# Kernel optimization log

Measured on AMD Instinct MI355X. Metric: run time of the kernel, lower is better.

The kernel has to match this reference:

```python
import jax, jax.numpy as jnp
import numpy as np
from jax import lax


def setup_inputs() -> dict:
    key = jax.random.key(0)
    ks = jax.random.split(key, 9)
    B, C, H, W = 32, 16, 128, 128
    x = jax.random.normal(ks[0], (B, C, H, W), dtype=jnp.float32)
    # sobel_x kernel as in source; the executed code leaves conv_sobel_x with tiled sobel_x.T
    sobel = jnp.array([[-1.0, 0.0, 1.0], [-2.0, 0.0, 2.0], [-1.0, 0.0, 1.0]], dtype=jnp.float32) / 8.0
    Wx = jnp.tile(sobel.T, (16, 16, 1, 1))  # [O=16, I=16, 3, 3]
    bx = jax.random.normal(ks[1], (16,), dtype=jnp.float32) * 0.05
    # conv_sobel_y retained its default (random) init in the source; model as random params
    Wy = jax.random.normal(ks[2], (16, 16, 3, 3), dtype=jnp.float32) * (1.0 / np.sqrt(16 * 9))
    by = jax.random.normal(ks[3], (16,), dtype=jnp.float32) * 0.05
    W1 = jax.random.normal(ks[4], (128, 48), dtype=jnp.float32) * (1.0 / np.sqrt(48))
    b1 = jax.random.normal(ks[5], (128,), dtype=jnp.float32) * 0.01
    W2 = jax.random.normal(ks[6], (16, 128), dtype=jnp.float32) * (1.0 / np.sqrt(128))
    b2 = jax.random.normal(ks[7], (16,), dtype=jnp.float32) * 0.01
    return {"x": x, "Wx": Wx, "bx": bx, "Wy": Wy, "by": by,
            "W1": W1, "b1": b1, "W2": W2, "b2": b2}


def _conv_same(x, w, b):
    # x: [B,C,H,W], w: [O,I,3,3] -> [B,O,H,W]
    y = lax.conv_general_dilated(x, w, window_strides=(1, 1), padding="SAME",
                                 dimension_numbers=("NCHW", "OIHW", "NCHW"))
    return y + b[None, :, None, None]


def reference(x, Wx, bx, Wy, by, W1, b1, W2, b2):
    # concat along channels: [B, 48, H, W]
    feat = jnp.concatenate([_conv_same(x, Wx, bx), _conv_same(x, Wy, by), x], axis=1)
    # torch transpose(1, 3): [B, W, H, 48]
    feat = jnp.transpose(feat, (0, 3, 2, 1))
    h = jax.nn.relu(jnp.einsum("bwhc,oc->bwho", feat, W1) + b1)
    out = jnp.einsum("bwhc,oc->bwho", h, W2) + b2  # [B, W, H, 16]
    return out
```

## Files before the change

### kernel.cpp

```cpp
#include <hip/hip_runtime.h>
#include <hip/hip_bf16.h>

typedef __hip_bfloat16 bf16;
typedef __attribute__((ext_vector_type(8))) short short8;
typedef __attribute__((ext_vector_type(4))) short short4v;
typedef __attribute__((ext_vector_type(4))) float float4v;

#define TH 16
#define TW 8
#define HALO_H 18
#define HALO_W 10
#define CS 24
#define KS 136

#define W2B_EL 20480
#define WSF_BYTE 45056

__global__ void prep(const float* __restrict__ Wx, const float* __restrict__ bx,
                     const float* __restrict__ Wy, const float* __restrict__ by,
                     const float* __restrict__ W1, const float* __restrict__ b1,
                     const float* __restrict__ W2, const float* __restrict__ b2,
                     bf16* __restrict__ wsb, float* __restrict__ wsf) {
    int t = blockIdx.x * blockDim.x + threadIdx.x;
    int stride = gridDim.x * blockDim.x;
    for (int f = t; f < 128 * 160; f += stride) {
        int j = f / 160, k = f - j * 160;
        int g = k >> 4, c = k & 15;
        float v = 0.0f;
        if (g < 9) {
            for (int o = 0; o < 16; ++o) {
                float wx = Wx[(o * 16 + c) * 9 + g];
                float wy = Wy[(o * 16 + c) * 9 + g];
                v = fmaf(W1[j * 48 + o], wx, v);
                v = fmaf(W1[j * 48 + 16 + o], wy, v);
            }
            if (g == 4) v += W1[j * 48 + 32 + c];
        }
        wsb[f] = __float2bfloat16(v);
    }
    for (int f = t; f < 2048; f += stride) wsb[W2B_EL + f] = __float2bfloat16(W2[f]);
    for (int j = t; j < 128; j += stride) {
        float v = b1[j];
        for (int o = 0; o < 16; ++o) {
            v = fmaf(W1[j * 48 + o], bx[o], v);
            v = fmaf(W1[j * 48 + 16 + o], by[o], v);
        }
        wsf[j] = v;
    }
    if (t < 16) wsf[128 + t] = b2[t];
}

__global__ __launch_bounds__(256, 2) void nca_mfma(const float* __restrict__ x,
                                                   const bf16* __restrict__ wsb,
                                                   const float* __restrict__ wsf,
                                                   float* __restrict__ out,
                                                   int gridTiles) {
    __shared__ bf16 xs[HALO_W * HALO_H * CS];
    __shared__ bf16 hs[128 * KS];

    const int tid = threadIdx.x;
    const int wave = tid >> 6;
    const int lane = tid & 63;
    const int hl = lane & 15;
    const int quad = lane >> 4;
    const int r0 = quad * 4;
    const int mgrp = wave >> 1;
    const int ngrp = wave & 1;

    short8 afrag[4][5];
#pragma unroll
    for (int mt = 0; mt < 4; ++mt) {
        int m = mgrp * 64 + mt * 16 + hl;
#pragma unroll
        for (int q = 0; q < 5; ++q)
            afrag[mt][q] = *(const short8*)(wsb + m * 160 + q * 32 + quad * 8);
    }
    short8 w2frag[4];
#pragma unroll
    for (int r = 0; r < 4; ++r)
        w2frag[r] = *(const short8*)(wsb + W2B_EL + hl * 128 + r * 32 + quad * 8);
    float b1r[4][4];
#pragma unroll
    for (int mt = 0; mt < 4; ++mt)
#pragma unroll
        for (int r = 0; r < 4; ++r) b1r[mt][r] = wsf[mgrp * 64 + mt * 16 + r0 + r];
    float b2r[4];
#pragma unroll
    for (int r = 0; r < 4; ++r) b2r[r] = wsf[128 + r0 + r];

    for (int t = blockIdx.x; t < 4096; t += gridTiles) {
        int b = t >> 7;
        int rem = t & 127;
        int wt = rem >> 3, ht = rem & 7;
        int h0 = ht * 16, w0 = wt * 8;

        __syncthreads();

        const float* xb = x + (size_t)b * 16 * 128 * 128;
        for (int f = tid; f < 16 * HALO_H * HALO_W; f += 256) {
            int c = f / (HALO_H * HALO_W);
            int rr = f - c * (HALO_H * HALO_W);
            int hh = rr / HALO_W;
            int ww = rr - hh * HALO_W;
            int gh = h0 - 1 + hh, gw = w0 - 1 + ww;
            float v = 0.0f;
            if ((unsigned)gh < 128u && (unsigned)gw < 128u)
                v = xb[(c * 128 + gh) * 128 + gw];
            xs[(ww * HALO_H + hh) * CS + c] = __float2bfloat16(v);
        }
        __syncthreads();

        float4v acc[4][4];
#pragma unroll
        for (int mt = 0; mt < 4; ++mt)
#pragma unroll
            for (int nt = 0; nt < 4; ++nt) acc[mt][nt] = (float4v)0.0f;

#pragma unroll
        for (int q = 0; q < 5; ++q) {
            int g = q * 2 + (quad >> 1);
            if (g > 8) g = 8;
            int kh = g / 3, kw = g - kh * 3;
            int c0 = (quad & 1) * 8;
            short8 bfrag[4];
#pragma unroll
            for (int nt = 0; nt < 4; ++nt) {
                int ww = ngrp * 4 + nt + kw;
                bfrag[nt] = *(const short8*)(xs + (ww * HALO_H + hl + kh) * CS + c0);
            }
#pragma unroll
            for (int nt = 0; nt < 4; ++nt)
#pragma unroll
                for (int mt = 0; mt < 4; ++mt)
                    acc[mt][nt] = __builtin_amdgcn_mfma_f32_16x16x32_bf16(
                        afrag[mt][q], bfrag[nt], acc[mt][nt], 0, 0, 0);
        }

#pragma unroll
        for (int mt = 0; mt < 4; ++mt)
#pragma unroll
            for (int nt = 0; nt < 4; ++nt) {
                int p = (ngrp * 4 + nt) * 16 + hl;
                int m = mgrp * 64 + mt * 16 + r0;
                short4v pk;
#pragma unroll
                for (int r = 0; r < 4; ++r) {
                    float v = acc[mt][nt][r] + b1r[mt][r];
                    v = fmaxf(v, 0.0f);
                    bf16 hb = __float2bfloat16(v);
                    pk[r] = *reinterpret_cast<short*>(&hb);
                }
                *(short4v*)(hs + p * KS + m) = pk;
            }
        __syncthreads();

        float4v acc2[2];
        acc2[0] = (float4v)0.0f;
        acc2[1] = (float4v)0.0f;
#pragma unroll
        for (int r = 0; r < 4; ++r) {
#pragma unroll
            for (int i = 0; i < 2; ++i) {
                int p = (wave * 2 + i) * 16 + hl;
                short8 bfrag = *(const short8*)(hs + p * KS + r * 32 + quad * 8);
                acc2[i] = __builtin_amdgcn_mfma_f32_16x16x32_bf16(
                    w2frag[r], bfrag, acc2[i], 0, 0, 0);
            }
        }

#pragma unroll
        for (int i = 0; i < 2; ++i) {
            int nt = wave * 2 + i;
            size_t ofs = (((size_t)b * 128 + (w0 + nt)) * 128 + (h0 + hl)) * 16 + r0;
            float4 v = make_float4(acc2[i][0] + b2r[0], acc2[i][1] + b2r[1],
                                   acc2[i][2] + b2r[2], acc2[i][3] + b2r[3]);
            *(float4*)(out + ofs) = v;
        }
    }
}

extern "C" void kernel_launch(void* const* d_in, const int* in_sizes, int n_in,
                              void* d_out, int out_size, void* d_ws, size_t ws_size,
                              hipStream_t stream) {
    const float* x  = (const float*)d_in[0];
    const float* Wx = (const float*)d_in[1];
    const float* bx = (const float*)d_in[2];
    const float* Wy = (const float*)d_in[3];
    const float* by = (const float*)d_in[4];
    const float* W1 = (const float*)d_in[5];
    const float* b1 = (const float*)d_in[6];
    const float* W2 = (const float*)d_in[7];
    const float* b2 = (const float*)d_in[8];
    bf16* wsb = (bf16*)d_ws;
    float* wsf = (float*)((char*)d_ws + WSF_BYTE);
    float* out = (float*)d_out;

    hipLaunchKernelGGL(prep, dim3(80), dim3(256), 0, stream,
                       Wx, bx, Wy, by, W1, b1, W2, b2, wsb, wsf);
    const int grid = 1024;
    hipLaunchKernelGGL(nca_mfma, dim3(grid), dim3(256), 0, stream,
                       x, wsb, wsf, out, grid);
}
```

Measured before the change: 149.6 us.

## Pre-transpose input to channel-last bf16 and double-buffer halo loads

Adds a pre-pass that converts x from NCHW fp32 into a channel-last bf16 buffer in workspace, so each halo pixel's 16 channels become two 16-byte vector loads instead of 16 scattered fp32 loads. The main kernel prefetches the next tile's halo into registers while computing the current one, writes it into a double-buffered shared-memory tile, and raises occupancy to 3 blocks per CU with a larger grid. This costs an extra full read and write of x in the pre-pass plus more workspace, and the old path is kept as a fallback when workspace is too small.

```diff
diff --git a/kernel.cpp b/kernel.cpp
--- a/kernel.cpp
+++ b/kernel.cpp
@@ -6,23 +6,49 @@
 typedef __attribute__((ext_vector_type(4))) short short4v;
 typedef __attribute__((ext_vector_type(4))) float float4v;
 
-#define TH 16
-#define TW 8
 #define HALO_H 18
 #define HALO_W 10
 #define CS 24
 #define KS 136
+#define XS_EL (HALO_W * HALO_H * CS)
 
 #define W2B_EL 20480
 #define WSF_BYTE 45056
-
-__global__ void prep(const float* __restrict__ Wx, const float* __restrict__ bx,
-                     const float* __restrict__ Wy, const float* __restrict__ by,
-                     const float* __restrict__ W1, const float* __restrict__ b1,
-                     const float* __restrict__ W2, const float* __restrict__ b2,
-                     bf16* __restrict__ wsb, float* __restrict__ wsf) {
-    int t = blockIdx.x * blockDim.x + threadIdx.x;
-    int stride = gridDim.x * blockDim.x;
+#define XT_BYTE 65536
+
+__device__ __forceinline__ unsigned int bfbits(float f) {
+    bf16 h = __float2bfloat16(f);
+    unsigned short u;
+    __builtin_memcpy(&u, &h, 2);
+    return (unsigned int)u;
+}
+
+__global__ void prep_all(const float* __restrict__ x,
+                         const float* __restrict__ Wx, const float* __restrict__ bx,
+                         const float* __restrict__ Wy, const float* __restrict__ by,
+                         const float* __restrict__ W1, const float* __restrict__ b1,
+                         const float* __restrict__ W2, const float* __restrict__ b2,
+                         bf16* __restrict__ wsb, float* __restrict__ wsf,
+                         bf16* __restrict__ xT, int tb) {
+    int blk = blockIdx.x;
+    int tid = threadIdx.x;
+    if (blk < tb) {
+        int b = blk >> 7;
+        int w = tid >> 1, half = tid & 1;
+        const float* src = x + (((size_t)(b * 16 + half * 8)) * 128 + (blk & 127)) * 128 + w;
+        unsigned int pk[4];
+#pragma unroll
+        for (int i = 0; i < 4; ++i) {
+            unsigned int lo = bfbits(src[(size_t)(2 * i) * 16384]);
+            unsigned int hi = bfbits(src[(size_t)(2 * i + 1) * 16384]);
+            pk[i] = lo | (hi << 16);
+        }
+        *(uint4*)(xT + ((size_t)blk * 128 + w) * 16 + half * 8) =
+            make_uint4(pk[0], pk[1], pk[2], pk[3]);
+        return;
+    }
+    int t = (blk - tb) * 256 + tid;
+    int stride = 80 * 256;
     for (int f = t; f < 128 * 160; f += stride) {
         int j = f / 160, k = f - j * 160;
         int g = k >> 4, c = k & 15;
@@ -50,11 +76,170 @@
     if (t < 16) wsf[128 + t] = b2[t];
 }
 
-__global__ __launch_bounds__(256, 2) void nca_mfma(const float* __restrict__ x,
-                                                   const bf16* __restrict__ wsb,
-                                                   const float* __restrict__ wsf,
-                                                   float* __restrict__ out,
-                                                   int gridTiles) {
+__global__ __launch_bounds__(256, 3) void nca_mfma_t(const bf16* __restrict__ xT,
+                                                     const bf16* __restrict__ wsb,
+                                                     const float* __restrict__ wsf,
+                                                     float* __restrict__ out,
+                                                     int gridTiles) {
+    __shared__ __align__(16) bf16 xs[2][XS_EL];
+    __shared__ __align__(16) bf16 hs[128 * KS];
+
+    const int tid = threadIdx.x;
+    const int wave = tid >> 6;
+    const int lane = tid & 63;
+    const int hl = lane & 15;
+    const int quad = lane >> 4;
+    const int r0 = quad * 4;
+    const int mgrp = wave >> 1;
+    const int ngrp = wave & 1;
+
+    short8 afrag[4][5];
+#pragma unroll
+    for (int mt = 0; mt < 4; ++mt) {
+        int m = mgrp * 64 + mt * 16 + hl;
+#pragma unroll
+        for (int q = 0; q < 5; ++q)
+            afrag[mt][q] = *(const short8*)(wsb + m * 160 + q * 32 + quad * 8);
+    }
+    short8 w2frag[4];
+#pragma unroll
+    for (int r = 0; r < 4; ++r)
+        w2frag[r] = *(const short8*)(wsb + W2B_EL + hl * 128 + r * 32 + quad * 8);
+    float b1r[4][4];
+#pragma unroll
+    for (int mt = 0; mt < 4; ++mt)
+#pragma unroll
+        for (int r = 0; r < 4; ++r) b1r[mt][r] = wsf[mgrp * 64 + mt * 16 + r0 + r];
+    float b2r[4];
+#pragma unroll
+    for (int r = 0; r < 4; ++r) b2r[r] = wsf[128 + r0 + r];
+
+    const int hh0 = tid / 20, rr0 = tid % 20;
+    const int sww0 = rr0 >> 1, shf0 = rr0 & 1;
+    const int f1 = tid + 256;
+    const int hh1 = f1 / 20, rr1 = f1 % 20;
+    const int sww1 = rr1 >> 1, shf1 = rr1 & 1;
+    const bool has1 = (tid < 104);
+
+    uint4 pre0, pre1;
+
+#define LOAD_TILE(T)                                                                  \
+    {                                                                                 \
+        int b_ = (T) >> 7, rem_ = (T) & 127;                                          \
+        int w0_ = (rem_ >> 3) * 8, h0_ = (rem_ & 7) * 16;                             \
+        {                                                                             \
+            int gh = h0_ - 1 + hh0, gw = w0_ - 1 + sww0;                              \
+            bool ok = ((unsigned)gh < 128u) && ((unsigned)gw < 128u);                 \
+            long off = (((long)b_ << 14) + gh * 128 + gw) * 16 + (shf0 << 3);         \
+            const uint4* p = (const uint4*)(xT + (ok ? off : 0));                     \
+            uint4 v = *p;                                                             \
+            if (!ok) { v.x = 0; v.y = 0; v.z = 0; v.w = 0; }                          \
+            pre0 = v;                                                                 \
+        }                                                                             \
+        if (has1) {                                                                   \
+            int gh = h0_ - 1 + hh1, gw = w0_ - 1 + sww1;                              \
+            bool ok = ((unsigned)gh < 128u) && ((unsigned)gw < 128u);                 \
+            long off = (((long)b_ << 14) + gh * 128 + gw) * 16 + (shf1 << 3);         \
+            const uint4* p = (const uint4*)(xT + (ok ? off : 0));                     \
+            uint4 v = *p;                                                             \
+            if (!ok) { v.x = 0; v.y = 0; v.z = 0; v.w = 0; }                          \
+            pre1 = v;                                                                 \
+        }                                                                             \
+    }
+
+    int t = blockIdx.x;
+    LOAD_TILE(t);
+    int buf = 0;
+
+    for (; t < 4096; t += gridTiles) {
+        const int b = t >> 7;
+        const int rem = t & 127;
+        const int w0 = (rem >> 3) * 8;
+        const int h0 = (rem & 7) * 16;
+
+        *(uint4*)(&xs[buf][(sww0 * HALO_H + hh0) * CS + shf0 * 8]) = pre0;
+        if (has1) *(uint4*)(&xs[buf][(sww1 * HALO_H + hh1) * CS + shf1 * 8]) = pre1;
+        __syncthreads();
+
+        int tn = t + gridTiles;
+        if (tn < 4096) LOAD_TILE(tn);
+
+        float4v acc[4][4];
+#pragma unroll
+        for (int mt = 0; mt < 4; ++mt)
+#pragma unroll
+            for (int nt = 0; nt < 4; ++nt) acc[mt][nt] = (float4v)0.0f;
+
+#pragma unroll
+        for (int q = 0; q < 5; ++q) {
+            int g = q * 2 + (quad >> 1);
+            if (g > 8) g = 8;
+            int kh = g / 3, kw = g - kh * 3;
+            int c0 = (quad & 1) * 8;
+            short8 bfrag[4];
+#pragma unroll
+            for (int nt = 0; nt < 4; ++nt) {
+                int ww = ngrp * 4 + nt + kw;
+                bfrag[nt] = *(const short8*)(&xs[buf][(ww * HALO_H + hl + kh) * CS + c0]);
+            }
+#pragma unroll
+            for (int nt = 0; nt < 4; ++nt)
+#pragma unroll
+                for (int mt = 0; mt < 4; ++mt)
+                    acc[mt][nt] = __builtin_amdgcn_mfma_f32_16x16x32_bf16(
+                        afrag[mt][q], bfrag[nt], acc[mt][nt], 0, 0, 0);
+        }
+
+#pragma unroll
+        for (int mt = 0; mt < 4; ++mt)
+#pragma unroll
+            for (int nt = 0; nt < 4; ++nt) {
+                int p = (ngrp * 4 + nt) * 16 + hl;
+                int m = mgrp * 64 + mt * 16 + r0;
+                short4v pk;
+#pragma unroll
+                for (int r = 0; r < 4; ++r) {
+                    float v = acc[mt][nt][r] + b1r[mt][r];
+                    v = fmaxf(v, 0.0f);
+                    bf16 hb = __float2bfloat16(v);
+                    pk[r] = *reinterpret_cast<short*>(&hb);
+                }
+                *(short4v*)(hs + p * KS + m) = pk;
+            }
+        __syncthreads();
+
+        float4v acc2[2];
+        acc2[0] = (float4v)0.0f;
+        acc2[1] = (float4v)0.0f;
+#pragma unroll
+        for (int r = 0; r < 4; ++r) {
+#pragma unroll
+            for (int i = 0; i < 2; ++i) {
+                int p = (wave * 2 + i) * 16 + hl;
+                short8 bfrag = *(const short8*)(hs + p * KS + r * 32 + quad * 8);
+                acc2[i] = __builtin_amdgcn_mfma_f32_16x16x32_bf16(
+                    w2frag[r], bfrag, acc2[i], 0, 0, 0);
+            }
+        }
+
+#pragma unroll
+        for (int i = 0; i < 2; ++i) {
+            int nt = wave * 2 + i;
+            size_t ofs = (((size_t)b * 128 + (w0 + nt)) * 128 + (h0 + hl)) * 16 + r0;
+            float4 v = make_float4(acc2[i][0] + b2r[0], acc2[i][1] + b2r[1],
+                                   acc2[i][2] + b2r[2], acc2[i][3] + b2r[3]);
+            *(float4*)(out + ofs) = v;
+        }
+        buf ^= 1;
+    }
+#undef LOAD_TILE
+}
+
+__global__ __launch_bounds__(256, 2) void nca_mfma_fb(const float* __restrict__ x,
+                                                      const bf16* __restrict__ wsb,
+                                                      const float* __restrict__ wsf,
+                                                      float* __restrict__ out,
+                                                      int gridTiles) {
     __shared__ bf16 xs[HALO_W * HALO_H * CS];
     __shared__ bf16 hs[128 * KS];
 
@@ -193,11 +378,22 @@
     const float* b2 = (const float*)d_in[8];
     bf16* wsb = (bf16*)d_ws;
     float* wsf = (float*)((char*)d_ws + WSF_BYTE);
+    bf16* xT = (bf16*)((char*)d_ws + XT_BYTE);
     float* out = (float*)d_out;
 
-    hipLaunchKernelGGL(prep, dim3(80), dim3(256), 0, stream,
-                       Wx, bx, Wy, by, W1, b1, W2, b2, wsb, wsf);
-    const int grid = 1024;
-    hipLaunchKernelGGL(nca_mfma, dim3(grid), dim3(256), 0, stream,
-                       x, wsb, wsf, out, grid);
-}
+    const size_t need = (size_t)XT_BYTE + (size_t)32 * 128 * 128 * 16 * 2;
+    const bool big = ws_size >= need;
+    const int tb = big ? 4096 : 0;
+
+    hipLaunchKernelGGL(prep_all, dim3(tb + 80), dim3(256), 0, stream,
+                       x, Wx, bx, Wy, by, W1, b1, W2, b2, wsb, wsf, xT, tb);
+    if (big) {
+        const int grid = 1536;
+        hipLaunchKernelGGL(nca_mfma_t, dim3(grid), dim3(256), 0, stream,
+                           xT, wsb, wsf, out, grid);
+    } else {
+        const int grid = 1024;
+        hipLaunchKernelGGL(nca_mfma_fb, dim3(grid), dim3(256), 0, stream,
+                           x, wsb, wsf, out, grid);
+    }
+}
```

New measurement: 202.7 us. 1.35x slower.
